# Performance work log

Hardware: AMD Instinct MI355X
Metric: run time of the kernel (lower is better)

The kernel has to match this reference:

```python
import jax, jax.numpy as jnp
import numpy as np

SEQ, BATCH, D_MODEL = 1536, 2, 1024
N_HEAD, D_HEAD, N_ROLL = 16, 64, 3
SCALE = 1.0 / float(np.sqrt(D_HEAD))
EPS_DENOM = 1e-5
EPS_LN = 1e-5


def _dpfp(x, n_roll=N_ROLL):
    # relu feature map: cat(relu(x), relu(-x)), then roll-multiply expansion
    x = jnp.concatenate([jax.nn.relu(x), jax.nn.relu(-x)], axis=-1)  # [S,B,N,2D]
    return jnp.concatenate(
        [x * jnp.roll(x, shift=i, axis=-1) for i in range(1, n_roll + 1)], axis=-1
    )  # [S,B,N,2D*n_roll]


def setup_inputs() -> dict:
    key = jax.random.key(0)
    k_h, k_q, k_kv, k_o = jax.random.split(key, 4)
    std = 1.0 / float(np.sqrt(D_MODEL))
    h = jax.random.normal(k_h, (SEQ, BATCH, D_MODEL), jnp.float32)
    Wq = jax.random.normal(k_q, (N_HEAD * D_HEAD, D_MODEL), jnp.float32) * std
    Wkv = jax.random.normal(k_kv, (2 * N_HEAD * D_HEAD, D_MODEL), jnp.float32) * std
    Wo = jax.random.normal(k_o, (D_MODEL, N_HEAD * D_HEAD), jnp.float32) * std
    ln_gamma = jnp.ones((D_MODEL,), jnp.float32)
    ln_beta = jnp.zeros((D_MODEL,), jnp.float32)
    # Transformer-XL causal mask: triu(ones(qlen, klen), 1)[:, :, None] -> dim 3
    attn_mask = jnp.triu(jnp.ones((SEQ, SEQ), bool), k=1)[:, :, None]
    return {"h": h, "Wq": Wq, "Wkv": Wkv, "Wo": Wo,
            "ln_gamma": ln_gamma, "ln_beta": ln_beta, "attn_mask": attn_mask}


def reference(h, Wq, Wkv, Wo, ln_gamma, ln_beta, attn_mask):
    S, B, _ = h.shape
    # projections (no mems, post-lnorm, eval mode -> dropout identity)
    q = (h @ Wq.T).reshape(S, B, N_HEAD, D_HEAD)
    k, v = jnp.split(h @ Wkv.T, 2, axis=-1)
    k = k.reshape(S, B, N_HEAD, D_HEAD)
    v = v.reshape(S, B, N_HEAD, D_HEAD)
    # DPFP feature maps -> feature dim 2*D_HEAD*N_ROLL
    q = _dpfp(q)
    k = _dpfp(k)
    # kernelized scores [S,S,B,N]
    score = jnp.einsum('ibnd,jbnd->ijbn', q, k) * SCALE
    # 3-D mask [qlen,klen,1] -> broadcast over (b via size-1) and heads
    score = jnp.where(attn_mask[:, :, :, None], 0.0, score)
    # sum-normalization over keys (axis 1 = j)
    denom = jnp.sum(score, axis=1, keepdims=True) + EPS_DENOM
    prob = score / denom
    attn_vec = jnp.einsum('ijbn,jbnd->ibnd', prob, v).reshape(S, B, N_HEAD * D_HEAD)
    attn_out = attn_vec @ Wo.T
    # post-layernorm residual
    x = h + attn_out
    mean = jnp.mean(x, axis=-1, keepdims=True)
    var = jnp.var(x, axis=-1, keepdims=True)
    return ln_gamma * (x - mean) / jnp.sqrt(var + EPS_LN) + ln_beta
```

## Files before the change

kernel.cpp:

```cpp
#include <hip/hip_runtime.h>
#include <hip/hip_bf16.h>

#define S_LEN 1536
#define BATCH 2
#define DMODEL 1024
#define NHEAD 16
#define DHEAD 64
#define FDIM 384
#define CHUNK 64
#define NCHUNK 24
#define ROWS (S_LEN*BATCH)
#define SCALE_F 0.125f
#define EPS_D 1e-5f
#define EPS_LN 1e-5f

typedef unsigned short u16;
typedef __attribute__((ext_vector_type(8))) __bf16 bf16x8;
typedef __attribute__((ext_vector_type(8))) unsigned short ushort8;
typedef __attribute__((ext_vector_type(4))) float f32x4;

static __device__ __forceinline__ float bf2f(u16 a) {
  return __uint_as_float(((unsigned)a) << 16);
}
static __device__ __forceinline__ u16 f2bf(float x) {
  unsigned u = __float_as_uint(x);
  unsigned r = (u + 0x7FFFu + ((u >> 16) & 1u)) >> 16;
  return (u16)r;
}
static __device__ __forceinline__ void gload_lds16(const void* g, void* l) {
  __builtin_amdgcn_global_load_lds(
      (const __attribute__((address_space(1))) void*)g,
      (__attribute__((address_space(3))) void*)l, 16, 0, 0);
}
#define MFMA(a, b, c) __builtin_amdgcn_mfma_f32_16x16x32_bf16(a, b, c, 0, 0, 0)


__global__ __launch_bounds__(256) void cvt_all(
    const float* __restrict__ h, const float* __restrict__ Wq,
    const float* __restrict__ Wkv, const float* __restrict__ Wo,
    u16* __restrict__ h_bf, u16* __restrict__ Wqkv_bf, u16* __restrict__ Wo_bf) {
  int i = blockIdx.x * 256 + threadIdx.x;
  const float* src; u16* dst; int j;
  if (i < 786432) { src = h; dst = h_bf; j = i; }
  else if (i < 1048576) { src = Wq; dst = Wqkv_bf; j = i - 786432; }
  else if (i < 1572864) { src = Wkv; dst = Wqkv_bf + 1048576; j = i - 1048576; }
  else { src = Wo; dst = Wo_bf; j = i - 1572864; }
  float4 v = ((const float4*)src)[j];
  ushort4 o = {f2bf(v.x), f2bf(v.y), f2bf(v.z), f2bf(v.w)};
  ((ushort4*)dst)[j] = o;
}

__global__ __launch_bounds__(256) void gemm_qkv_bf16(
    const u16* __restrict__ A, const u16* __restrict__ B,
    u16* __restrict__ C, int M, int N, int K) {
  __shared__ u16 As[128 * 32];
  __shared__ u16 Bs[128 * 32];
  const int t = threadIdx.x;
  const int l = t & 63, w = t >> 6;
  const int nbx = gridDim.x;
  const int fl = blockIdx.y * nbx + blockIdx.x;
  const int q8 = (nbx * gridDim.y) >> 3;
  const int fl2 = (fl & 7) * q8 + (fl >> 3);
  const int m0 = (fl2 / nbx) * 128, n0 = (fl2 % nbx) * 128;
  const int wm = (w >> 1) * 64, wn = (w & 1) * 64;

  f32x4 acc[4][4];
#pragma unroll
  for (int i = 0; i < 4; ++i)
#pragma unroll
    for (int j = 0; j < 4; ++j) acc[i][j] = (f32x4)0.f;

  const size_t Kb = (size_t)K * 2;
  const int o_lo = w * 1024 + l * 16;
  const int o_hi = 4096 + w * 1024 + l * 16;
  const int r_lo = o_lo >> 6, kb_lo = o_lo & 63;
  const int r_hi = o_hi >> 6, kb_hi = o_hi & 63;

  const char* Ap0 = (const char*)A + (size_t)(m0 + r_lo) * Kb + kb_lo;
  const char* Ap1 = (const char*)A + (size_t)(m0 + r_hi) * Kb + kb_hi;
  const char* Bp0 = (const char*)B + (size_t)(n0 + r_lo) * Kb + kb_lo;
  const char* Bp1 = (const char*)B + (size_t)(n0 + r_hi) * Kb + kb_hi;
  u16* AsB0 = As + (w * 1024) / 2;
  u16* AsB1 = As + (4096 + w * 1024) / 2;
  u16* BsB0 = Bs + (w * 1024) / 2;
  u16* BsB1 = Bs + (4096 + w * 1024) / 2;

  const int fr = l & 15, ko = (l >> 4) * 8;

  for (int k0 = 0; k0 < K; k0 += 32) {
    __syncthreads();
    gload_lds16(Ap0, AsB0);
    gload_lds16(Ap1, AsB1);
    gload_lds16(Bp0, BsB0);
    gload_lds16(Bp1, BsB1);
    Ap0 += 64; Ap1 += 64; Bp0 += 64; Bp1 += 64;
    __syncthreads();
    bf16x8 a[4], b[4];
#pragma unroll
    for (int m = 0; m < 4; ++m)
      a[m] = *(const bf16x8*)&As[(wm + m * 16 + fr) * 32 + ko];
#pragma unroll
    for (int n = 0; n < 4; ++n)
      b[n] = *(const bf16x8*)&Bs[(wn + n * 16 + fr) * 32 + ko];
#pragma unroll
    for (int m = 0; m < 4; ++m)
#pragma unroll
      for (int n = 0; n < 4; ++n)
        acc[m][n] = MFMA(a[m], b[n], acc[m][n]);
  }

  const int cr = (l >> 4) * 4, ccol = l & 15;
#pragma unroll
  for (int m = 0; m < 4; ++m)
#pragma unroll
    for (int n = 0; n < 4; ++n)
#pragma unroll
      for (int j = 0; j < 4; ++j)
        C[(size_t)(m0 + wm + m * 16 + cr + j) * N + (n0 + wn + n * 16 + ccol)] =
            f2bf(acc[m][n][j]);
}

__global__ __launch_bounds__(256) void gemm64_bf16(
    const u16* __restrict__ A, const u16* __restrict__ B,
    float* __restrict__ C, int M, int N, int K) {
  __shared__ u16 As[64 * 32];
  __shared__ u16 Bs[64 * 32];
  const int t = threadIdx.x;
  const int l = t & 63, w = t >> 6;
  const int nbx = gridDim.x;
  const int fl = blockIdx.y * nbx + blockIdx.x;
  const int q8 = (nbx * gridDim.y) >> 3;
  const int fl2 = (fl & 7) * q8 + (fl >> 3);
  const int m0 = (fl2 / nbx) * 64, n0 = (fl2 % nbx) * 64;
  const int fr = l & 15, kg = l >> 4;
  const size_t Kb = (size_t)K * 2;
  const int o = t * 16, r = o >> 6, kb = o & 63;
  const char* Ap = (const char*)A + (size_t)(m0 + r) * Kb + kb;
  const char* Bp = (const char*)B + (size_t)(n0 + r) * Kb + kb;
  u16* AsB = As + (w * 1024) / 2;
  u16* BsB = Bs + (w * 1024) / 2;
  f32x4 acc[4];
#pragma unroll
  for (int i = 0; i < 4; ++i) acc[i] = (f32x4)0.f;
  for (int k0 = 0; k0 < K; k0 += 32) {
    __syncthreads();
    gload_lds16(Ap, AsB);
    gload_lds16(Bp, BsB);
    Ap += 64; Bp += 64;
    __syncthreads();
    bf16x8 a = *(const bf16x8*)&As[(16 * w + fr) * 32 + kg * 8];
#pragma unroll
    for (int nt = 0; nt < 4; ++nt) {
      bf16x8 b = *(const bf16x8*)&Bs[(16 * nt + fr) * 32 + kg * 8];
      acc[nt] = MFMA(a, b, acc[nt]);
    }
  }
#pragma unroll
  for (int nt = 0; nt < 4; ++nt)
#pragma unroll
    for (int reg = 0; reg < 4; ++reg)
      C[(size_t)(m0 + 16 * w + 4 * kg + reg) * N + (n0 + 16 * nt + fr)] =
          acc[nt][reg];
}

__global__ __launch_bounds__(256) void dpfp_q64(
    const u16* __restrict__ proj, u16* __restrict__ qft) {
  const int c = blockIdx.x, bn = blockIdx.y;
  const int b = bn >> 4, n = bn & 15;
  const int s0 = c * CHUNK;
  const int t = threadIdx.x;
  __shared__ float y[64][129];
  const int j = t >> 2, dq = (t & 3) << 4;
  const u16* qp = proj + (size_t)((s0 + j) * BATCH + b) * 3072 + n * DHEAD + dq;
#pragma unroll
  for (int u = 0; u < 2; ++u) {
    ushort8 xv = *(const ushort8*)(qp + 8 * u);
#pragma unroll
    for (int e = 0; e < 8; ++e) {
      float x = bf2f(xv[e]);
      int d = dq + 8 * u + e;
      y[j][d] = fmaxf(x, 0.f);
      y[j][64 + d] = fmaxf(-x, 0.f);
    }
  }
  __syncthreads();
  u16* base = qft + (size_t)bn * 589824;
  const int fr = t & 15, kg = (t >> 4) & 3, l = t & 63;
#pragma unroll 2
  for (int it = 0; it < 12; ++it) {
    int tile = it * 4 + (t >> 6);
    int rT = tile / 12, cB = tile % 12;
    int sl = rT * 16 + fr;
    ushort8 o;
#pragma unroll
    for (int e = 0; e < 8; ++e) {
      int f = cB * 32 + kg * 8 + e, m = f & 127, sh = (f >> 7) + 1;
      o[e] = f2bf(y[sl][m] * y[sl][(m - sh) & 127]);
    }
    *(ushort8*)(base + ((size_t)(4 * c + rT) * 12 + cB) * 512 + l * 8) = o;
  }
}

__global__ __launch_bounds__(256) void dpfp_k64(
    const u16* __restrict__ proj, u16* __restrict__ kft,
    u16* __restrict__ kfTt, u16* __restrict__ vTt) {
  const int c = blockIdx.x, bn = blockIdx.y;
  const int b = bn >> 4, n = bn & 15;
  const int s0 = c * CHUNK;
  const int t = threadIdx.x;
  __shared__ float y[64][129];
  __shared__ float vs[64][65];
  const int j = t >> 2, dq = (t & 3) << 4;
  const u16* kp = proj + (size_t)((s0 + j) * BATCH + b) * 3072 + n * DHEAD + dq;
#pragma unroll
  for (int u = 0; u < 2; ++u) {
    ushort8 xv = *(const ushort8*)(kp + 1024 + 8 * u);
    ushort8 vv = *(const ushort8*)(kp + 2048 + 8 * u);
#pragma unroll
    for (int e = 0; e < 8; ++e) {
      float x = bf2f(xv[e]);
      int d = dq + 8 * u + e;
      y[j][d] = fmaxf(x, 0.f);
      y[j][64 + d] = fmaxf(-x, 0.f);
      vs[j][d] = bf2f(vv[e]);
    }
  }
  __syncthreads();
  const int fr = t & 15, kg = (t >> 4) & 3, l = t & 63;
  {
    u16* base = kft + (size_t)bn * 589824;
#pragma unroll 2
    for (int it = 0; it < 12; ++it) {
      int tile = it * 4 + (t >> 6);
      int rT = tile / 12, cB = tile % 12;
      int sl = rT * 16 + fr;
      ushort8 o;
#pragma unroll
      for (int e = 0; e < 8; ++e) {
        int f = cB * 32 + kg * 8 + e, m = f & 127, sh = (f >> 7) + 1;
        o[e] = f2bf(y[sl][m] * y[sl][(m - sh) & 127]);
      }
      *(ushort8*)(base + ((size_t)(4 * c + rT) * 12 + cB) * 512 + l * 8) = o;
    }
  }
  {
    u16* base = kfTt + (size_t)bn * 589824;
#pragma unroll 2
    for (int it = 0; it < 12; ++it) {
      int tile = it * 4 + (t >> 6);
      int rT = tile >> 1, cHalf = tile & 1;
      int f = rT * 16 + fr, m = f & 127, sh = (f >> 7) + 1;
      int sb = cHalf * 32 + kg * 8;
      ushort8 o;
#pragma unroll
      for (int e = 0; e < 8; ++e)
        o[e] = f2bf(y[sb + e][m] * y[sb + e][(m - sh) & 127]);
      *(ushort8*)(base + ((size_t)rT * 48 + 2 * c + cHalf) * 512 + l * 8) = o;
    }
  }
  {
    u16* base = vTt + (size_t)bn * 98304;
#pragma unroll
    for (int it = 0; it < 2; ++it) {
      int tile = it * 4 + (t >> 6);
      int rT = tile >> 1, cHalf = tile & 1;
      int d = rT * 16 + fr;
      int sb = cHalf * 32 + kg * 8;
      ushort8 o;
#pragma unroll
      for (int e = 0; e < 8; ++e) o[e] = f2bf(vs[sb + e][d]);
      *(ushort8*)(base + ((size_t)rT * 48 + 2 * c + cHalf) * 512 + l * 8) = o;
    }
  }
}

__global__ __launch_bounds__(256) void chunk_kv_scan(
    const u16* __restrict__ kfTt, const u16* __restrict__ vTt,
    u16* __restrict__ kvswz, float* __restrict__ ksumst) {
  const int fl = blockIdx.x;
  const int fl2 = (fl & 7) * 48 + (fl >> 3);
  const int bn = fl2 / 12, ft2 = fl2 % 12;
  const int t = threadIdx.x, l = t & 63, w = t >> 6;
  const int fr = l & 15, kg = l >> 4;
  const u16* vt_base = vTt + (size_t)bn * 98304;
  const u16* kt_base = kfTt + (size_t)bn * 589824;

  __shared__ u16 Ys[64][40];

  f32x4 pacc0 = (f32x4)0.f, pacc1 = (f32x4)0.f;
  float pks = 0.f;

  for (int c = 0; c < NCHUNK; ++c) {
    f32x4 acc0 = (f32x4)0.f, acc1 = (f32x4)0.f;
    float ksp = 0.f;
#pragma unroll
    for (int ksi = 0; ksi < 2; ++ksi) {
      bf16x8 a = *(const bf16x8*)(vt_base + ((size_t)w * 48 + 2 * c + ksi) * 512 + l * 8);
      const u16* bp0 = kt_base + ((size_t)(2 * ft2 + 0) * 48 + 2 * c + ksi) * 512 + l * 8;
      const u16* bp1 = kt_base + ((size_t)(2 * ft2 + 1) * 48 + 2 * c + ksi) * 512 + l * 8;
      bf16x8 b0 = *(const bf16x8*)bp0;
      bf16x8 b1 = *(const bf16x8*)bp1;
      if (w == 0) {
        ushort8 raw = *(const ushort8*)bp0;
#pragma unroll
        for (int e = 0; e < 8; ++e) ksp += bf2f(raw[e]);
      } else if (w == 1) {
        ushort8 raw = *(const ushort8*)bp1;
#pragma unroll
        for (int e = 0; e < 8; ++e) ksp += bf2f(raw[e]);
      }
      acc0 = MFMA(a, b0, acc0);
      acc1 = MFMA(a, b1, acc1);
    }
    __syncthreads();
#pragma unroll
    for (int reg = 0; reg < 4; ++reg) {
      Ys[16 * w + 4 * kg + reg][fr] = f2bf(pacc0[reg]);
      Ys[16 * w + 4 * kg + reg][16 + fr] = f2bf(pacc1[reg]);
    }
    __syncthreads();
    {
      ushort8 o = *(const ushort8*)&Ys[w * 16 + fr][kg * 8];
      *(ushort8*)(kvswz + (size_t)(bn * NCHUNK + c) * 24576 +
                  (size_t)(w * 12 + ft2) * 512 + l * 8) = o;
    }
    if (w < 2) {
      float x = ksp;
      x += __shfl_xor(x, 16);
      x += __shfl_xor(x, 32);
      if (kg == 0)
        ksumst[(size_t)(bn * NCHUNK + c) * FDIM + ft2 * 32 + w * 16 + fr] = pks;
      pks += x;
    }
    pacc0 += acc0;
    pacc1 += acc1;
  }
}

__global__ __launch_bounds__(256) void attn_mfma(
    const u16* __restrict__ qft, const u16* __restrict__ kft,
    const u16* __restrict__ vTt, const u16* __restrict__ kvswz,
    const float* __restrict__ kspre, u16* __restrict__ attnvec) {
  const int c = blockIdx.x, bn = blockIdx.y;
  const int b = bn >> 4, n = bn & 15;
  const int s0 = c * CHUNK;
  const int t = threadIdx.x, l = t & 63, w = t >> 6;
  const int fr = l & 15, kg = l >> 4;

  const u16* qbase = qft + (size_t)bn * 589824;
  const u16* kbase = kft + (size_t)bn * 589824;
  const u16* vbase = vTt + (size_t)bn * 98304;
  const u16* kvbase = kvswz + (size_t)(bn * NCHUNK + c) * 24576;
  const float* ksp = kspre + (size_t)(bn * NCHUNK + c) * FDIM;

  __shared__ u16 Sb[64][70];

  f32x4 acc[9];
#pragma unroll
  for (int i = 0; i < 9; ++i) acc[i] = (f32x4)0.f;

#pragma unroll 3
  for (int cB = 0; cB < 12; ++cB) {
    bf16x8 a = *(const bf16x8*)(qbase + ((size_t)(4 * c + w) * 12 + cB) * 512 + l * 8);
#pragma unroll
    for (int nt = 0; nt < 4; ++nt) {
      bf16x8 bfrag = *(const bf16x8*)(kbase + ((size_t)(4 * c + nt) * 12 + cB) * 512 + l * 8);
      acc[nt] = MFMA(a, bfrag, acc[nt]);
    }
#pragma unroll
    for (int nt = 0; nt < 4; ++nt) {
      bf16x8 bfrag = *(const bf16x8*)(kvbase + ((size_t)nt * 12 + cB) * 512 + l * 8);
      acc[4 + nt] = MFMA(a, bfrag, acc[4 + nt]);
    }
    ushort8 bd = {0, 0, 0, 0, 0, 0, 0, 0};
    if (fr == 0) {
#pragma unroll
      for (int e = 0; e < 8; ++e) bd[e] = f2bf(ksp[cB * 32 + kg * 8 + e]);
    }
    union { ushort8 u; bf16x8 v; } cu;
    cu.u = bd;
    acc[8] = MFMA(a, cu.v, acc[8]);
  }

  float rsum[4];
#pragma unroll
  for (int reg = 0; reg < 4; ++reg) {
    int i = 16 * w + 4 * kg + reg;
    float r = 0.f;
#pragma unroll
    for (int nt = 0; nt < 4; ++nt) {
      int jj = 16 * nt + fr;
      float sval = (jj <= i) ? acc[nt][reg] : 0.f;
      acc[nt][reg] = sval;
      r += sval;
    }
    r += __shfl_xor(r, 1); r += __shfl_xor(r, 2);
    r += __shfl_xor(r, 4); r += __shfl_xor(r, 8);
    rsum[reg] = r;
  }
#pragma unroll
  for (int nt = 0; nt < 4; ++nt)
#pragma unroll
    for (int reg = 0; reg < 4; ++reg)
      Sb[16 * w + 4 * kg + reg][16 * nt + fr] = f2bf(acc[nt][reg]);

  __syncthreads();

#pragma unroll
  for (int ksi = 0; ksi < 2; ++ksi) {
    const int ko = ksi * 32 + kg * 8;
    bf16x8 a = *(const bf16x8*)&Sb[16 * w + fr][ko];
#pragma unroll
    for (int nt = 0; nt < 4; ++nt) {
      bf16x8 bfrag = *(const bf16x8*)(vbase + ((size_t)nt * 48 + 2 * c + ksi) * 512 + l * 8);
      acc[4 + nt] = MFMA(a, bfrag, acc[4 + nt]);
    }
  }

#pragma unroll
  for (int reg = 0; reg < 4; ++reg) {
    int i = 16 * w + 4 * kg + reg;
    float dinter = __shfl(acc[8][reg], l & 48);
    float den = rsum[reg] + dinter;
    float sc = SCALE_F / (SCALE_F * den + EPS_D);
    int rowg = (s0 + i) * BATCH + b;
    u16* orow = attnvec + (size_t)rowg * DMODEL + n * DHEAD;
#pragma unroll
    for (int nt = 0; nt < 4; ++nt)
      orow[16 * nt + fr] = f2bf(acc[4 + nt][reg] * sc);
  }
}

__global__ __launch_bounds__(256) void ln_kernel(
    const float* __restrict__ h, const float* __restrict__ ao,
    const float* __restrict__ gamma, const float* __restrict__ beta,
    float* __restrict__ out) {
  const int r = blockIdx.x, t = threadIdx.x;
  const float* hr = h + (size_t)r * DMODEL;
  const float* ar = ao + (size_t)r * DMODEL;
  float4 xh = *(const float4*)(hr + t * 4);
  float4 xa = *(const float4*)(ar + t * 4);
  float4 x = {xh.x + xa.x, xh.y + xa.y, xh.z + xa.z, xh.w + xa.w};
  float sum = x.x + x.y + x.z + x.w;
  float sq = x.x * x.x + x.y * x.y + x.z * x.z + x.w * x.w;
#pragma unroll
  for (int o = 32; o >= 1; o >>= 1) {
    sum += __shfl_xor(sum, o);
    sq += __shfl_xor(sq, o);
  }
  __shared__ float s_sum[4], s_sq[4];
  int w = t >> 6;
  if ((t & 63) == 0) { s_sum[w] = sum; s_sq[w] = sq; }
  __syncthreads();
  sum = s_sum[0] + s_sum[1] + s_sum[2] + s_sum[3];
  sq = s_sq[0] + s_sq[1] + s_sq[2] + s_sq[3];
  float mean = sum * (1.0f / DMODEL);
  float var = sq * (1.0f / DMODEL) - mean * mean;
  float rstd = rsqrtf(var + EPS_LN);
  float4 g = *(const float4*)(gamma + t * 4);
  float4 bb = *(const float4*)(beta + t * 4);
  float4 o4 = {g.x * (x.x - mean) * rstd + bb.x,
               g.y * (x.y - mean) * rstd + bb.y,
               g.z * (x.z - mean) * rstd + bb.z,
               g.w * (x.w - mean) * rstd + bb.w};
  *(float4*)(out + (size_t)r * DMODEL + t * 4) = o4;
}

extern "C" void kernel_launch(void* const* d_in, const int* in_sizes, int n_in,
                              void* d_out, int out_size, void* d_ws, size_t ws_size,
                              hipStream_t stream) {
  const float* h = (const float*)d_in[0];
  const float* Wq = (const float*)d_in[1];
  const float* Wkv = (const float*)d_in[2];
  const float* Wo = (const float*)d_in[3];
  const float* gamma = (const float*)d_in[4];
  const float* beta = (const float*)d_in[5];
  float* out = (float*)d_out;

  u16* proj = (u16*)d_ws;
  u16* qft = proj + 9437184;
  u16* kft = qft + 18874368;
  u16* kfTt = kft + 18874368;
  u16* vTt = kfTt + 18874368;
  u16* kvswz = vTt + 3145728;
  float* ksumst = (float*)(kvswz + 18874368);
  u16* Wo_bf = (u16*)(ksumst + 294912);
  u16* h_bf = Wo_bf + 1048576;
  u16* Wqkv_bf = h_bf + 3145728;
  u16* attnvec = Wqkv_bf + 3145728;
  float* attnout = (float*)(attnvec + 3145728);

  hipLaunchKernelGGL(cvt_all, dim3(7168), dim3(256), 0, stream,
                     h, Wq, Wkv, Wo, h_bf, Wqkv_bf, Wo_bf);
  hipLaunchKernelGGL(gemm_qkv_bf16, dim3(24, 24), dim3(256), 0, stream,
                     h_bf, Wqkv_bf, proj, ROWS, 3072, 1024);
  hipLaunchKernelGGL(dpfp_q64, dim3(24, 32), dim3(256), 0, stream, proj, qft);
  hipLaunchKernelGGL(dpfp_k64, dim3(24, 32), dim3(256), 0, stream,
                     proj, kft, kfTt, vTt);
  hipLaunchKernelGGL(chunk_kv_scan, dim3(384), dim3(256), 0, stream,
                     kfTt, vTt, kvswz, ksumst);
  hipLaunchKernelGGL(attn_mfma, dim3(24, 32), dim3(256), 0, stream,
                     qft, kft, vTt, kvswz, ksumst, attnvec);
  hipLaunchKernelGGL(gemm64_bf16, dim3(16, 48), dim3(256), 0, stream,
                     attnvec, Wo_bf, attnout, ROWS, 1024, 1024);
  hipLaunchKernelGGL(ln_kernel, dim3(3072), dim3(256), 0, stream,
                     h, attnout, gamma, beta, out);
}
```

Baseline: 148.0 us.

## Fuse DPFP query feature map into attention kernel and store Wo output as bf16

Removes the dpfp_q64 kernel and its 37MB qft intermediate by building the relu-split query in LDS inside attn_mfma. Each MFMA A-fragment of roll-product features is then formed on the fly from packed bf16 words. Separately, the output projection GEMM now writes bf16 instead of fp32, and the layernorm reads bf16, halving that intermediate's traffic. The cost is some extra ALU work in the attention loop and reduced precision on the attention output before the residual add.

```diff
diff --git a/kernel.cpp b/kernel.cpp
--- a/kernel.cpp
+++ b/kernel.cpp
@@ -33,6 +33,45 @@
       (__attribute__((address_space(3))) void*)l, 16, 0, 0);
 }
 #define MFMA(a, b, c) __builtin_amdgcn_mfma_f32_16x16x32_bf16(a, b, c, 0, 0, 0)
+
+static __device__ __forceinline__ void unpk(unsigned u, float& lo, float& hi) {
+  lo = __uint_as_float(u << 16);
+  hi = __uint_as_float(u & 0xffff0000u);
+}
+
+static __device__ __forceinline__ bf16x8 feat_frag(
+    const u16* __restrict__ yrow, int m, int SH) {
+  union U { ushort8 v; unsigned u[4]; };
+  U y1, y0;
+  y1.v = *(const ushort8*)(yrow + m);
+  y0.v = *(const ushort8*)(yrow + ((m - 8) & 127));
+  unsigned seq2 = y0.u[2], seq3 = y0.u[3];
+  unsigned seq4 = y1.u[0], seq5 = y1.u[1], seq6 = y1.u[2], seq7 = y1.u[3];
+  unsigned y2u[4];
+  if (SH == 2) {
+    y2u[0] = seq3; y2u[1] = seq4; y2u[2] = seq5; y2u[3] = seq6;
+  } else if (SH == 1) {
+    y2u[0] = (seq3 >> 16) | (seq4 << 16);
+    y2u[1] = (seq4 >> 16) | (seq5 << 16);
+    y2u[2] = (seq5 >> 16) | (seq6 << 16);
+    y2u[3] = (seq6 >> 16) | (seq7 << 16);
+  } else {
+    y2u[0] = (seq2 >> 16) | (seq3 << 16);
+    y2u[1] = (seq3 >> 16) | (seq4 << 16);
+    y2u[2] = (seq4 >> 16) | (seq5 << 16);
+    y2u[3] = (seq5 >> 16) | (seq6 << 16);
+  }
+  bf16x8 out;
+#pragma unroll
+  for (int i = 0; i < 4; ++i) {
+    float a0, a1, b0, b1;
+    unpk(y1.u[i], a0, a1);
+    unpk(y2u[i], b0, b1);
+    out[2 * i] = (__bf16)(a0 * b0);
+    out[2 * i + 1] = (__bf16)(a1 * b1);
+  }
+  return out;
+}
 
 
 __global__ __launch_bounds__(256) void cvt_all(
@@ -122,7 +161,7 @@
 
 __global__ __launch_bounds__(256) void gemm64_bf16(
     const u16* __restrict__ A, const u16* __restrict__ B,
-    float* __restrict__ C, int M, int N, int K) {
+    u16* __restrict__ C, int M, int N, int K) {
   __shared__ u16 As[64 * 32];
   __shared__ u16 Bs[64 * 32];
   const int t = threadIdx.x;
@@ -160,45 +199,7 @@
 #pragma unroll
     for (int reg = 0; reg < 4; ++reg)
       C[(size_t)(m0 + 16 * w + 4 * kg + reg) * N + (n0 + 16 * nt + fr)] =
-          acc[nt][reg];
-}
-
-__global__ __launch_bounds__(256) void dpfp_q64(
-    const u16* __restrict__ proj, u16* __restrict__ qft) {
-  const int c = blockIdx.x, bn = blockIdx.y;
-  const int b = bn >> 4, n = bn & 15;
-  const int s0 = c * CHUNK;
-  const int t = threadIdx.x;
-  __shared__ float y[64][129];
-  const int j = t >> 2, dq = (t & 3) << 4;
-  const u16* qp = proj + (size_t)((s0 + j) * BATCH + b) * 3072 + n * DHEAD + dq;
-#pragma unroll
-  for (int u = 0; u < 2; ++u) {
-    ushort8 xv = *(const ushort8*)(qp + 8 * u);
-#pragma unroll
-    for (int e = 0; e < 8; ++e) {
-      float x = bf2f(xv[e]);
-      int d = dq + 8 * u + e;
-      y[j][d] = fmaxf(x, 0.f);
-      y[j][64 + d] = fmaxf(-x, 0.f);
-    }
-  }
-  __syncthreads();
-  u16* base = qft + (size_t)bn * 589824;
-  const int fr = t & 15, kg = (t >> 4) & 3, l = t & 63;
-#pragma unroll 2
-  for (int it = 0; it < 12; ++it) {
-    int tile = it * 4 + (t >> 6);
-    int rT = tile / 12, cB = tile % 12;
-    int sl = rT * 16 + fr;
-    ushort8 o;
-#pragma unroll
-    for (int e = 0; e < 8; ++e) {
-      int f = cB * 32 + kg * 8 + e, m = f & 127, sh = (f >> 7) + 1;
-      o[e] = f2bf(y[sl][m] * y[sl][(m - sh) & 127]);
-    }
-    *(ushort8*)(base + ((size_t)(4 * c + rT) * 12 + cB) * 512 + l * 8) = o;
-  }
+          f2bf(acc[nt][reg]);
 }
 
 __global__ __launch_bounds__(256) void dpfp_k64(
@@ -338,7 +339,7 @@
 }
 
 __global__ __launch_bounds__(256) void attn_mfma(
-    const u16* __restrict__ qft, const u16* __restrict__ kft,
+    const u16* __restrict__ proj, const u16* __restrict__ kft,
     const u16* __restrict__ vTt, const u16* __restrict__ kvswz,
     const float* __restrict__ kspre, u16* __restrict__ attnvec) {
   const int c = blockIdx.x, bn = blockIdx.y;
@@ -347,39 +348,66 @@
   const int t = threadIdx.x, l = t & 63, w = t >> 6;
   const int fr = l & 15, kg = l >> 4;
 
-  const u16* qbase = qft + (size_t)bn * 589824;
   const u16* kbase = kft + (size_t)bn * 589824;
   const u16* vbase = vTt + (size_t)bn * 98304;
   const u16* kvbase = kvswz + (size_t)(bn * NCHUNK + c) * 24576;
   const float* ksp = kspre + (size_t)(bn * NCHUNK + c) * FDIM;
 
+  __shared__ u16 y_q[64][132];
   __shared__ u16 Sb[64][70];
 
+  {
+    const int j = t >> 2, dq = (t & 3) << 4;
+    const u16* qp = proj + (size_t)((s0 + j) * BATCH + b) * 3072 + n * DHEAD + dq;
+#pragma unroll
+    for (int u = 0; u < 2; ++u) {
+      ushort8 xv = *(const ushort8*)(qp + 8 * u);
+      ushort8 pos, neg;
+#pragma unroll
+      for (int e = 0; e < 8; ++e) {
+        u16 x = xv[e];
+        bool sn = (x & 0x8000u) != 0;
+        pos[e] = sn ? (u16)0 : x;
+        neg[e] = sn ? (u16)(x & 0x7fffu) : (u16)0;
+      }
+      *(ushort8*)&y_q[j][dq + 8 * u] = pos;
+      *(ushort8*)&y_q[j][64 + dq + 8 * u] = neg;
+    }
+  }
+  __syncthreads();
+
   f32x4 acc[9];
 #pragma unroll
   for (int i = 0; i < 9; ++i) acc[i] = (f32x4)0.f;
 
-#pragma unroll 3
-  for (int cB = 0; cB < 12; ++cB) {
-    bf16x8 a = *(const bf16x8*)(qbase + ((size_t)(4 * c + w) * 12 + cB) * 512 + l * 8);
-#pragma unroll
-    for (int nt = 0; nt < 4; ++nt) {
-      bf16x8 bfrag = *(const bf16x8*)(kbase + ((size_t)(4 * c + nt) * 12 + cB) * 512 + l * 8);
-      acc[nt] = MFMA(a, bfrag, acc[nt]);
-    }
-#pragma unroll
-    for (int nt = 0; nt < 4; ++nt) {
-      bf16x8 bfrag = *(const bf16x8*)(kvbase + ((size_t)nt * 12 + cB) * 512 + l * 8);
-      acc[4 + nt] = MFMA(a, bfrag, acc[4 + nt]);
-    }
-    ushort8 bd = {0, 0, 0, 0, 0, 0, 0, 0};
-    if (fr == 0) {
-#pragma unroll
-      for (int e = 0; e < 8; ++e) bd[e] = f2bf(ksp[cB * 32 + kg * 8 + e]);
-    }
-    union { ushort8 u; bf16x8 v; } cu;
-    cu.u = bd;
-    acc[8] = MFMA(a, cu.v, acc[8]);
+  const u16* yqrow = &y_q[16 * w + fr][0];
+
+#pragma unroll
+  for (int shb = 0; shb < 3; ++shb) {
+#pragma unroll
+    for (int q4 = 0; q4 < 4; ++q4) {
+      const int cB = shb * 4 + q4;
+      const int m = q4 * 32 + kg * 8;
+      bf16x8 a = feat_frag(yqrow, m, shb + 1);
+#pragma unroll
+      for (int nt = 0; nt < 4; ++nt) {
+        bf16x8 bfrag = *(const bf16x8*)(kbase + ((size_t)(4 * c + nt) * 12 + cB) * 512 + l * 8);
+        acc[nt] = MFMA(a, bfrag, acc[nt]);
+      }
+#pragma unroll
+      for (int nt = 0; nt < 4; ++nt) {
+        bf16x8 bfrag = *(const bf16x8*)(kvbase + ((size_t)nt * 12 + cB) * 512 + l * 8);
+        acc[4 + nt] = MFMA(a, bfrag, acc[4 + nt]);
+      }
+      ushort8 bd = {0, 0, 0, 0, 0, 0, 0, 0};
+      if (fr == 0) {
+#pragma unroll
+        for (int e = 0; e < 8; ++e) bd[e] = f2bf(ksp[cB * 32 + kg * 8 + e]);
+      }
+      union { ushort8 u; bf16x8 v; } cu;
+      cu.u = bd;
+      acc[8] = MFMA(a, cu.v, acc[8]);
+    }
   }
 
   float rsum[4];
@@ -432,15 +460,16 @@
 }
 
 __global__ __launch_bounds__(256) void ln_kernel(
-    const float* __restrict__ h, const float* __restrict__ ao,
+    const float* __restrict__ h, const u16* __restrict__ ao,
     const float* __restrict__ gamma, const float* __restrict__ beta,
     float* __restrict__ out) {
   const int r = blockIdx.x, t = threadIdx.x;
   const float* hr = h + (size_t)r * DMODEL;
-  const float* ar = ao + (size_t)r * DMODEL;
+  const u16* ar = ao + (size_t)r * DMODEL;
   float4 xh = *(const float4*)(hr + t * 4);
-  float4 xa = *(const float4*)(ar + t * 4);
-  float4 x = {xh.x + xa.x, xh.y + xa.y, xh.z + xa.z, xh.w + xa.w};
+  ushort4 xa = *(const ushort4*)(ar + t * 4);
+  float4 x = {xh.x + bf2f(xa.x), xh.y + bf2f(xa.y),
+              xh.z + bf2f(xa.z), xh.w + bf2f(xa.w)};
   float sum = x.x + x.y + x.z + x.w;
   float sq = x.x * x.x + x.y * x.y + x.z * x.z + x.w * x.w;
 #pragma unroll
@@ -478,8 +507,7 @@
   float* out = (float*)d_out;
 
   u16* proj = (u16*)d_ws;
-  u16* qft = proj + 9437184;
-  u16* kft = qft + 18874368;
+  u16* kft = proj + 9437184;
   u16* kfTt = kft + 18874368;
   u16* vTt = kfTt + 18874368;
   u16* kvswz = vTt + 3145728;
@@ -488,19 +516,18 @@
   u16* h_bf = Wo_bf + 1048576;
   u16* Wqkv_bf = h_bf + 3145728;
   u16* attnvec = Wqkv_bf + 3145728;
-  float* attnout = (float*)(attnvec + 3145728);
+  u16* attnout = attnvec + 3145728;
 
   hipLaunchKernelGGL(cvt_all, dim3(7168), dim3(256), 0, stream,
                      h, Wq, Wkv, Wo, h_bf, Wqkv_bf, Wo_bf);
   hipLaunchKernelGGL(gemm_qkv_bf16, dim3(24, 24), dim3(256), 0, stream,
                      h_bf, Wqkv_bf, proj, ROWS, 3072, 1024);
-  hipLaunchKernelGGL(dpfp_q64, dim3(24, 32), dim3(256), 0, stream, proj, qft);
   hipLaunchKernelGGL(dpfp_k64, dim3(24, 32), dim3(256), 0, stream,
                      proj, kft, kfTt, vTt);
   hipLaunchKernelGGL(chunk_kv_scan, dim3(384), dim3(256), 0, stream,
                      kfTt, vTt, kvswz, ksumst);
   hipLaunchKernelGGL(attn_mfma, dim3(24, 32), dim3(256), 0, stream,
-                     qft, kft, vTt, kvswz, ksumst, attnvec);
+                     proj, kft, vTt, kvswz, ksumst, attnvec);
   hipLaunchKernelGGL(gemm64_bf16, dim3(16, 48), dim3(256), 0, stream,
                      attnvec, Wo_bf, attnout, ROWS, 1024, 1024);
   hipLaunchKernelGGL(ln_kernel, dim3(3072), dim3(256), 0, stream,
```

New measurement: 149.6 us. Within noise of the previous version (+1.1%).
